# Performance work log

Measured on AMD Instinct MI355X. Metric: run time of the kernel, lower is better.

## Reference

```python
import jax, jax.numpy as jnp
import numpy as np

B, L, D, H = 2, 2048, 512, 8
DH = D // H
THRESHOLD = 0.1


def setup_inputs() -> dict:
    key = jax.random.key(0)
    ks = jax.random.split(key, 8)
    s = 0.02  # weight scale to keep activations sane
    return {
        "q_x": jax.random.normal(ks[0], (B, L, D), jnp.float32),
        "k_x": jax.random.normal(ks[1], (B, L, D), jnp.float32),
        "v_x": jax.random.normal(ks[2], (B, L, D), jnp.float32),
        "energy_coeffs": jax.random.normal(ks[3], (B, L, 16), jnp.float32),
        "Wq": jax.random.normal(ks[4], (D, D), jnp.float32) * s,
        "bq": jnp.zeros((D,), jnp.float32),
        "Wk": jax.random.normal(ks[5], (D, D), jnp.float32) * s,
        "bk": jnp.zeros((D,), jnp.float32),
        "Wv": jax.random.normal(ks[6], (D, D), jnp.float32) * s,
        "bv": jnp.zeros((D,), jnp.float32),
        "Wo": jax.random.normal(ks[7], (D, D), jnp.float32) * s,
        "bo": jnp.zeros((D,), jnp.float32),
    }


def reference(q_x, k_x, v_x, energy_coeffs, Wq, bq, Wk, bk, Wv, bv, Wo, bo):
    b, l, d = q_x.shape
    # QKV projections (torch Linear: x @ W.T + b), split heads -> [B,H,L,Dh]
    Q = (q_x @ Wq.T + bq).reshape(b, l, H, DH).transpose(0, 2, 1, 3)
    K = (k_x @ Wk.T + bk).reshape(b, -1, H, DH).transpose(0, 2, 1, 3)
    V = (v_x @ Wv.T + bv).reshape(b, -1, H, DH).transpose(0, 2, 1, 3)
    scores = jnp.einsum("bhqd,bhkd->bhqk", Q, K) / jnp.sqrt(jnp.float32(DH))
    # straight-through energy-based key mask
    energy = jnp.abs(energy_coeffs).mean(axis=-1)  # [B, Lk]
    soft = jax.nn.sigmoid((energy - THRESHOLD) * 10.0)
    hard = (energy > THRESHOLD).astype(q_x.dtype)
    mask_val = soft + jax.lax.stop_gradient(hard - soft)  # fwd=hard, grad=soft
    scores = scores + (1.0 - mask_val)[:, None, None, :] * (-1e9)
    attn = jax.nn.softmax(scores, axis=-1)
    out = jnp.einsum("bhqk,bhkd->bhqd", attn, V)
    out = out.transpose(0, 2, 1, 3).reshape(b, l, d)
    return out @ Wo.T + bo
```

## Files before the change

### kernel.cpp

```cpp
#include <hip/hip_runtime.h>
#include <stdint.h>

#define B_ 2
#define L_ 2048
#define D_ 512
#define H_ 8
#define DH_ 64

using frag8 = __attribute__((ext_vector_type(8))) short;
using bf4   = __attribute__((ext_vector_type(4))) short;
using f32x4 = __attribute__((ext_vector_type(4))) float;
using u32x4 = __attribute__((ext_vector_type(4))) unsigned int;

#define QSC 0.18033688011112042f

__device__ __forceinline__ unsigned short f2bf(float f) {
    unsigned int u = __float_as_uint(f);
    u += 0x7fffu + ((u >> 16) & 1u);
    return (unsigned short)(u >> 16);
}

__device__ __forceinline__ unsigned int cvtpk(float lo, float hi_) {
    unsigned int r;
    asm("v_cvt_pk_bf16_f32 %0, %1, %2" : "=v"(r) : "v"(lo), "v"(hi_));
    return r;
}

__device__ __forceinline__ void gl2lds16(const void* g, void* lds) {
    __builtin_amdgcn_global_load_lds((const __attribute__((address_space(1))) void*)g,
                                     (__attribute__((address_space(3))) void*)lds,
                                     16, 0, 0);
}

template<int N>
__device__ __forceinline__ void vmwait() {
    asm volatile("s_waitcnt vmcnt(%0)" :: "n"(N) : "memory");
}

__global__ __launch_bounds__(256) void cvt_mask_kernel(
    const float* __restrict__ qx, const float* __restrict__ kx, const float* __restrict__ vx,
    const float* __restrict__ Wq, const float* __restrict__ Wk, const float* __restrict__ Wv,
    const float* __restrict__ Wo, const float* __restrict__ ec,
    unsigned short* qb, unsigned short* kb, unsigned short* vb,
    unsigned short* wqb, unsigned short* wkb, unsigned short* wvb, unsigned short* wob,
    float* __restrict__ mk)
{
    const long NA = (long)B_ * L_ * D_;
    const long NW = (long)D_ * D_;
    const long total4 = (3 * NA + 4 * NW) / 4;
    long q4 = (long)blockIdx.x * 256 + threadIdx.x;
    if (q4 < total4) {
        long i = q4 * 4;
        const float* src; unsigned short* dst; long off;
        if (i < NA)            { src = qx; dst = qb; off = i; }
        else if (i < 2 * NA)   { src = kx; dst = kb; off = i - NA; }
        else if (i < 3 * NA)   { src = vx; dst = vb; off = i - 2 * NA; }
        else {
            long j = i - 3 * NA;
            int w = (int)(j / NW);
            off = j - (long)w * NW;
            src = (w == 0) ? Wq : (w == 1) ? Wk : (w == 2) ? Wv : Wo;
            dst = (w == 0) ? wqb : (w == 1) ? wkb : (w == 2) ? wvb : wob;
        }
        float4 v = *(const float4*)(src + off);
        ushort4 o;
        o.x = f2bf(v.x); o.y = f2bf(v.y); o.z = f2bf(v.z); o.w = f2bf(v.w);
        *(ushort4*)(dst + off) = o;
    } else {
        long i = q4 - total4;
        if (i < B_ * L_) {
            const float4* p4 = (const float4*)(ec + i * 16);
            float s = 0.0f;
#pragma unroll
            for (int j = 0; j < 4; ++j) {
                float4 v = p4[j];
                s += fabsf(v.x) + fabsf(v.y) + fabsf(v.z) + fabsf(v.w);
            }
            float energy = s * (1.0f / 16.0f);
            mk[i] = (energy > 0.1f) ? 0.0f : -1.0e9f;
        }
    }
}

struct GemmArgs { const unsigned short* A; const unsigned short* W;
                  const float* bias; void* C; int mode; };

template<int BM, int BN>
__global__ __launch_bounds__(256) void gemm_kernel(GemmArgs a0, GemmArgs a1, GemmArgs a2,
                                                   int M, int N, int K)
{
    const int nwg = gridDim.x * gridDim.y * gridDim.z;
    int flat = blockIdx.x + gridDim.x * (blockIdx.y + gridDim.y * blockIdx.z);
    int swz  = (flat & 7) * (nwg >> 3) + (flat >> 3);
    const int bx = swz % gridDim.x;
    int t2 = swz / gridDim.x;
    const int by = t2 % gridDim.y;
    const int bz = t2 / gridDim.y;

    GemmArgs ga = bz == 0 ? a0 : (bz == 1 ? a1 : a2);
    const unsigned short* __restrict__ A = ga.A;
    const unsigned short* __restrict__ W = ga.W;
    const float* __restrict__ bias = ga.bias;

    constexpr int MF = BM / 32;
    constexpr int NF = BN / 32;
    constexpr int NL = BM / 32 + BN / 32;

    __shared__ __align__(16) unsigned short As[2][BM * 64];
    __shared__ __align__(16) unsigned short Bs[2][BN * 64];

    const int tid  = threadIdx.x;
    const int lane = tid & 63;
    const int wave = tid >> 6;
    const int hi   = lane >> 4;
    const int ln   = lane & 15;
    const int wr   = wave >> 1;
    const int wc   = wave & 1;

    const long mBase = (long)by * BM;
    const long nBase = (long)bx * BN;

    f32x4 acc[MF][NF];
#pragma unroll
    for (int m = 0; m < MF; ++m)
#pragma unroll
        for (int n = 0; n < NF; ++n) acc[m][n] = (f32x4){0.f, 0.f, 0.f, 0.f};

#define GSTAGE(KT, BUF) do {                                                    \
    _Pragma("unroll")                                                           \
    for (int i_ = 0; i_ < BM / 32; ++i_) {                                      \
        int cl_ = i_ * 256 + tid;                                               \
        int r_ = cl_ >> 3, c_ = cl_ & 7, s_ = c_ ^ (r_ & 7);                    \
        gl2lds16(A + (mBase + r_) * K + (KT) + s_ * 8, As[BUF] + cl_ * 8);      \
    }                                                                           \
    _Pragma("unroll")                                                           \
    for (int i_ = 0; i_ < BN / 32; ++i_) {                                      \
        int cl_ = i_ * 256 + tid;                                               \
        int r_ = cl_ >> 3, c_ = cl_ & 7, s_ = c_ ^ (r_ & 7);                    \
        gl2lds16(W + (nBase + r_) * K + (KT) + s_ * 8, Bs[BUF] + cl_ * 8);      \
    }                                                                           \
} while (0)

    GSTAGE(0, 0);

    const int nk = K / 64;
    for (int t = 0; t < nk; ++t) {
        const int buf = t & 1;
        if (t + 1 < nk) {
            GSTAGE((t + 1) * 64, buf ^ 1);
            vmwait<NL>();
        } else {
            vmwait<0>();
        }
        __builtin_amdgcn_s_barrier();
        __builtin_amdgcn_sched_barrier(0);

        frag8 af[2][MF], bfr[2][NF];
#pragma unroll
        for (int kk = 0; kk < 2; ++kk) {
#pragma unroll
            for (int m = 0; m < MF; ++m) {
                int row = wr * (BM / 2) + m * 16 + ln;
                int c = (kk * 4 + hi) ^ (row & 7);
                af[kk][m] = *(const frag8*)(As[buf] + row * 64 + c * 8);
            }
#pragma unroll
            for (int n = 0; n < NF; ++n) {
                int row = wc * (BN / 2) + n * 16 + ln;
                int c = (kk * 4 + hi) ^ (row & 7);
                bfr[kk][n] = *(const frag8*)(Bs[buf] + row * 64 + c * 8);
            }
        }
        __builtin_amdgcn_s_setprio(1);
#pragma unroll
        for (int kk = 0; kk < 2; ++kk)
#pragma unroll
            for (int m = 0; m < MF; ++m)
#pragma unroll
                for (int n = 0; n < NF; ++n)
                    acc[m][n] = __builtin_amdgcn_mfma_f32_16x16x32_bf16(af[kk][m], bfr[kk][n], acc[m][n], 0, 0, 0);
        __builtin_amdgcn_s_setprio(0);
        __builtin_amdgcn_sched_barrier(0);
        __builtin_amdgcn_s_barrier();
    }
#undef GSTAGE

    const int mode = ga.mode;
#pragma unroll
    for (int m = 0; m < MF; ++m) {
#pragma unroll
        for (int n = 0; n < NF; ++n) {
            long col = nBase + wc * (BN / 2) + n * 16 + ln;
            float bv = bias[col];
#pragma unroll
            for (int j = 0; j < 4; ++j) {
                long row = mBase + wr * (BM / 2) + m * 16 + hi * 4 + j;
                float v = acc[m][n][j] + bv;
                if (mode == 3) {
                    ((float*)ga.C)[row * N + col] = v;
                } else if (mode == 2) {
                    int dh = (int)col & 63;
                    int swv = ((dh & 7) << 1) | ((dh >> 3) & 1);
                    long nt = (row & ~63L) | (long)(((((int)(row >> 2)) & 15) ^ swv) << 2) | (row & 3);
                    ((unsigned short*)ga.C)[col * (long)(B_ * L_) + nt] = f2bf(v);
                } else {
                    if (mode == 1) v *= QSC;
                    ((unsigned short*)ga.C)[row * N + col] = f2bf(v);
                }
            }
        }
    }
}

__global__ __launch_bounds__(512, 4) void attn_kernel(
    const unsigned short* __restrict__ Qg, const unsigned short* __restrict__ Kg,
    const unsigned short* __restrict__ Vt, const float* __restrict__ mkg,
    unsigned short* __restrict__ Og)
{
    const int tid  = threadIdx.x;
    const int lane = tid & 63;
    const int wave = tid >> 6;
    const int grp  = wave >> 2;
    const int wq   = wave & 3;
    const int gtid = tid & 255;
    const int hi   = lane >> 4;
    const int ln   = lane & 15;

    const int bh = blockIdx.y;
    const int b  = bh >> 3, h = bh & 7;
    const unsigned short* Qb = Qg + ((long)b * L_) * D_ + h * DH_;
    const unsigned short* Kb = Kg + ((long)b * L_) * D_ + h * DH_;
    const unsigned short* Vb = Vt + (long)(h * DH_) * (B_ * L_) + (long)b * L_;
    const float* mkb = mkg + (long)b * L_;

    __shared__ __align__(16) char smem[65536];
    unsigned short* KsG = (unsigned short*)(smem + grp * 32768);
    unsigned short* VsG = (unsigned short*)(smem + grp * 32768 + 16384);

    const int q0 = blockIdx.x * 64 + wq * 16;

    frag8 qf[2];
#pragma unroll
    for (int ks = 0; ks < 2; ++ks)
        qf[ks] = *(const frag8*)(Qb + (long)(q0 + ln) * D_ + ks * 32 + hi * 8);

    const int sw  = ((ln & 7) << 1) | ((ln >> 3) & 1);
    const int sl0 = ((hi     ) ^ sw) << 2;
    const int sl1 = ((hi + 4 ) ^ sw) << 2;
    const int sl2 = ((hi + 8 ) ^ sw) << 2;
    const int sl3 = ((hi + 12) ^ sw) << 2;

#define STAGE(TT, BUF) do {                                                     \
    _Pragma("unroll")                                                           \
    for (int c2_ = 0; c2_ < 2; ++c2_) {                                         \
        int cl_ = c2_ * 256 + gtid;                                             \
        int r_ = cl_ >> 3, c_ = cl_ & 7;                                        \
        gl2lds16(Kb + (long)((TT) * 64 + r_) * D_ + ((c_ ^ (r_ & 7)) << 3),     \
                 KsG + (BUF) * 4096 + cl_ * 8);                                 \
        gl2lds16(Vb + (long)r_ * (B_ * L_) + (TT) * 64 + (c_ << 3),             \
                 VsG + (BUF) * 4096 + cl_ * 8);                                 \
    }                                                                           \
} while (0)

    STAGE(grp, 0);

    f32x4 o[4];
#pragma unroll
    for (int g = 0; g < 4; ++g) o[g] = (f32x4){0.f, 0.f, 0.f, 0.f};
    float m_run = -__builtin_inff();
    float l_run = 0.0f;

    for (int i = 0; i < 16; ++i) {
        const int T = 2 * i + grp;
        const int buf = i & 1;

        float4 m40 = *(const float4*)(mkb + T * 64 +      4 * hi);
        float4 m41 = *(const float4*)(mkb + T * 64 + 16 + 4 * hi);
        float4 m42 = *(const float4*)(mkb + T * 64 + 32 + 4 * hi);
        float4 m43 = *(const float4*)(mkb + T * 64 + 48 + 4 * hi);
        __builtin_amdgcn_sched_barrier(0);

        if (i < 15) {
            STAGE(2 * (i + 1) + grp, buf ^ 1);
            vmwait<8>();
        } else {
            vmwait<4>();
        }
        __builtin_amdgcn_s_barrier();
        __builtin_amdgcn_sched_barrier(0);

        const unsigned short* Kl = KsG + buf * 4096;
        const unsigned short* Vl = VsG + buf * 4096;

        f32x4 sv[4];
#pragma unroll
        for (int sh = 0; sh < 4; ++sh) sv[sh] = (f32x4){0.f, 0.f, 0.f, 0.f};
        __builtin_amdgcn_s_setprio(1);
#pragma unroll
        for (int sh = 0; sh < 4; ++sh) {
            int key = sh * 16 + ln;
#pragma unroll
            for (int ks = 0; ks < 2; ++ks) {
                frag8 kf = *(const frag8*)(Kl + key * 64 + (((ks * 4 + hi) ^ (ln & 7)) << 3));
                sv[sh] = __builtin_amdgcn_mfma_f32_16x16x32_bf16(kf, qf[ks], sv[sh], 0, 0, 0);
            }
        }
        __builtin_amdgcn_s_setprio(0);

        float sc[16];
        sc[0]  = sv[0][0] + m40.x; sc[1]  = sv[0][1] + m40.y;
        sc[2]  = sv[0][2] + m40.z; sc[3]  = sv[0][3] + m40.w;
        sc[4]  = sv[1][0] + m41.x; sc[5]  = sv[1][1] + m41.y;
        sc[6]  = sv[1][2] + m41.z; sc[7]  = sv[1][3] + m41.w;
        sc[8]  = sv[2][0] + m42.x; sc[9]  = sv[2][1] + m42.y;
        sc[10] = sv[2][2] + m42.z; sc[11] = sv[2][3] + m42.w;
        sc[12] = sv[3][0] + m43.x; sc[13] = sv[3][1] + m43.y;
        sc[14] = sv[3][2] + m43.z; sc[15] = sv[3][3] + m43.w;

        float t0 = fmaxf(fmaxf(sc[0], sc[1]), sc[2]);
        float t1 = fmaxf(fmaxf(sc[3], sc[4]), sc[5]);
        float t2 = fmaxf(fmaxf(sc[6], sc[7]), sc[8]);
        float t3 = fmaxf(fmaxf(sc[9], sc[10]), sc[11]);
        float t4 = fmaxf(fmaxf(sc[12], sc[13]), sc[14]);
        float tmax = fmaxf(fmaxf(fmaxf(t0, t1), fmaxf(t2, t3)), fmaxf(t4, sc[15]));
        tmax = fmaxf(tmax, __shfl_xor(tmax, 16));
        tmax = fmaxf(tmax, __shfl_xor(tmax, 32));

        if (!__all(tmax <= m_run)) {
            float m_new = fmaxf(m_run, tmax);
            float alpha = __builtin_amdgcn_exp2f(m_run - m_new);
            float a0 = __shfl(alpha, 4 * hi + 0);
            float a1 = __shfl(alpha, 4 * hi + 1);
            float a2 = __shfl(alpha, 4 * hi + 2);
            float a3 = __shfl(alpha, 4 * hi + 3);
#pragma unroll
            for (int g = 0; g < 4; ++g) {
                o[g][0] *= a0; o[g][1] *= a1; o[g][2] *= a2; o[g][3] *= a3;
            }
            l_run *= alpha;
            m_run = m_new;
        }

        float p[16];
#pragma unroll
        for (int j = 0; j < 16; ++j) p[j] = __builtin_amdgcn_exp2f(sc[j] - m_run);
        float s01 = (p[0] + p[1]) + (p[2] + p[3]);
        float s23 = (p[4] + p[5]) + (p[6] + p[7]);
        float s45 = (p[8] + p[9]) + (p[10] + p[11]);
        float s67 = (p[12] + p[13]) + (p[14] + p[15]);
        float ps = (s01 + s23) + (s45 + s67);
        ps += __shfl_xor(ps, 16);
        ps += __shfl_xor(ps, 32);
        l_run += ps;

        union PU { u32x4 u; frag8 f; } p0u, p1u;
        p0u.u = (u32x4){cvtpk(p[0], p[1]),  cvtpk(p[2], p[3]),
                        cvtpk(p[4], p[5]),  cvtpk(p[6], p[7])};
        p1u.u = (u32x4){cvtpk(p[8], p[9]),  cvtpk(p[10], p[11]),
                        cvtpk(p[12], p[13]), cvtpk(p[14], p[15])};

        __builtin_amdgcn_s_setprio(1);
#pragma unroll
        for (int g = 0; g < 4; ++g) {
            int rowb = (g * 16 + ln) * 64;
            bf4 a0 = *(const bf4*)(Vl + rowb + sl0);
            bf4 a1 = *(const bf4*)(Vl + rowb + sl1);
            bf4 a2 = *(const bf4*)(Vl + rowb + sl2);
            bf4 a3 = *(const bf4*)(Vl + rowb + sl3);
            frag8 vf0 = __builtin_shufflevector(a0, a1, 0, 1, 2, 3, 4, 5, 6, 7);
            frag8 vf1 = __builtin_shufflevector(a2, a3, 0, 1, 2, 3, 4, 5, 6, 7);
            o[g] = __builtin_amdgcn_mfma_f32_16x16x32_bf16(p0u.f, vf0, o[g], 0, 0, 0);
            o[g] = __builtin_amdgcn_mfma_f32_16x16x32_bf16(p1u.f, vf1, o[g], 0, 0, 0);
        }
        __builtin_amdgcn_s_setprio(0);

        __builtin_amdgcn_sched_barrier(0);
        __builtin_amdgcn_s_barrier();
    }
#undef STAGE

    float* oX = (float*)smem;
    float* mX = (float*)(smem + 64 * 68 * 4);
    float* lX = mX + 64;

    if (grp == 1) {
#pragma unroll
        for (int g = 0; g < 4; ++g)
#pragma unroll
            for (int j = 0; j < 4; ++j)
                oX[(wq * 16 + 4 * hi + j) * 68 + g * 16 + ln] = o[g][j];
        if (hi == 0) { mX[wq * 16 + ln] = m_run; lX[wq * 16 + ln] = l_run; }
    }
    __syncthreads();
    if (grp == 0) {
#pragma unroll
        for (int j = 0; j < 4; ++j) {
            int q = 4 * hi + j;
            float mA = __shfl(m_run, q);
            float lA = __shfl(l_run, q);
            float mB = mX[wq * 16 + q];
            float lB = lX[wq * 16 + q];
            float mm = fmaxf(mA, mB);
            float aA = __builtin_amdgcn_exp2f(mA - mm);
            float aB = __builtin_amdgcn_exp2f(mB - mm);
            float inv = 1.0f / (lA * aA + lB * aB);
            aA *= inv; aB *= inv;
#pragma unroll
            for (int g = 0; g < 4; ++g) {
                float v = o[g][j] * aA + oX[(wq * 16 + q) * 68 + g * 16 + ln] * aB;
                long idx = ((long)b * L_ + q0 + q) * D_ + h * DH_ + g * 16 + ln;
                Og[idx] = f2bf(v);
            }
        }
    }
}

extern "C" void kernel_launch(void* const* d_in, const int* in_sizes, int n_in,
                              void* d_out, int out_size, void* d_ws, size_t ws_size,
                              hipStream_t stream)
{
    const float* qx = (const float*)d_in[0];
    const float* kx = (const float*)d_in[1];
    const float* vx = (const float*)d_in[2];
    const float* ec = (const float*)d_in[3];
    const float* Wq = (const float*)d_in[4];
    const float* bq = (const float*)d_in[5];
    const float* Wk = (const float*)d_in[6];
    const float* bk = (const float*)d_in[7];
    const float* Wv = (const float*)d_in[8];
    const float* bv = (const float*)d_in[9];
    const float* Wo = (const float*)d_in[10];
    const float* bo = (const float*)d_in[11];
    float* out = (float*)d_out;

    const long NA = (long)B_ * L_ * D_;
    const long NW = (long)D_ * D_;

    unsigned short* qb  = (unsigned short*)d_ws;
    unsigned short* kb  = qb + NA;
    unsigned short* vb  = kb + NA;
    unsigned short* wqb = vb + NA;
    unsigned short* wkb = wqb + NW;
    unsigned short* wvb = wkb + NW;
    unsigned short* wob = wvb + NW;
    unsigned short* Qp  = wob + NW;
    unsigned short* Kp  = Qp + NA;
    unsigned short* Vtp = Kp + NA;
    unsigned short* Ap  = qb;
    float*          mk  = (float*)(Vtp + NA);

    const long total4 = (3 * NA + 4 * NW) / 4;
    const long nblk = (total4 + B_ * L_ + 255) / 256;
    cvt_mask_kernel<<<dim3((unsigned)nblk), dim3(256), 0, stream>>>(
        qx, kx, vx, Wq, Wk, Wv, Wo, ec, qb, kb, vb, wqb, wkb, wvb, wob, mk);

    GemmArgs zq = {qb, wqb, bq, Qp, 1};
    GemmArgs zk = {kb, wkb, bk, Kp, 0};
    GemmArgs zv = {vb, wvb, bv, Vtp, 2};
    gemm_kernel<64, 128><<<dim3(4, 64, 3), dim3(256), 0, stream>>>(zq, zk, zv, B_ * L_, D_, D_);

    attn_kernel<<<dim3(L_ / 64, B_ * H_), dim3(512), 0, stream>>>(Qp, Kp, Vtp, mk, Ap);

    GemmArgs zo = {Ap, wob, bo, out, 3};
    gemm_kernel<64, 64><<<dim3(8, 64, 1), dim3(256), 0, stream>>>(zo, zo, zo, B_ * L_, D_, D_);
}
```

Baseline: 79.43 us.

## Drop split-KV groups in attention, use 256-thread blocks with lazy rescale

The attention kernel no longer splits keys between two 4-wave groups that are merged through LDS. Each 256-thread block now processes all 32 key tiles itself, using a 32KB double buffer and writing the normalized output directly. The V transpose swizzle is changed so each B fragment is fetched with two 16-byte LDS reads instead of four 8-byte reads. Max rescaling is now skipped unless the tile max exceeds the running max by more than 8, which trades a small risk of exp overflow for fewer rescales. The cost is twice as many serial iterations per block, offset by potentially higher occupancy and no final cross-group merge.

```diff
diff --git a/kernel.cpp b/kernel.cpp
--- a/kernel.cpp
+++ b/kernel.cpp
@@ -8,7 +8,6 @@
 #define DH_ 64
 
 using frag8 = __attribute__((ext_vector_type(8))) short;
-using bf4   = __attribute__((ext_vector_type(4))) short;
 using f32x4 = __attribute__((ext_vector_type(4))) float;
 using u32x4 = __attribute__((ext_vector_type(4))) unsigned int;
 
@@ -200,8 +199,10 @@
                     ((float*)ga.C)[row * N + col] = v;
                 } else if (mode == 2) {
                     int dh = (int)col & 63;
-                    int swv = ((dh & 7) << 1) | ((dh >> 3) & 1);
-                    long nt = (row & ~63L) | (long)(((((int)(row >> 2)) & 15) ^ swv) << 2) | (row & 3);
+                    int s  = ((int)row >> 2) & 15;
+                    int w  = (int)row & 3;
+                    int q  = ((((s & 3) << 2) | (s >> 2)) ^ ((dh & 7) << 1));
+                    long nt = (row & ~63L) | (long)(q << 2) | w;
                     ((unsigned short*)ga.C)[col * (long)(B_ * L_) + nt] = f2bf(v);
                 } else {
                     if (mode == 1) v *= QSC;
@@ -212,7 +213,7 @@
     }
 }
 
-__global__ __launch_bounds__(512, 4) void attn_kernel(
+__global__ __launch_bounds__(256, 5) void attn_kernel(
     const unsigned short* __restrict__ Qg, const unsigned short* __restrict__ Kg,
     const unsigned short* __restrict__ Vt, const float* __restrict__ mkg,
     unsigned short* __restrict__ Og)
@@ -220,9 +221,6 @@
     const int tid  = threadIdx.x;
     const int lane = tid & 63;
     const int wave = tid >> 6;
-    const int grp  = wave >> 2;
-    const int wq   = wave & 3;
-    const int gtid = tid & 255;
     const int hi   = lane >> 4;
     const int ln   = lane & 15;
 
@@ -233,36 +231,33 @@
     const unsigned short* Vb = Vt + (long)(h * DH_) * (B_ * L_) + (long)b * L_;
     const float* mkb = mkg + (long)b * L_;
 
-    __shared__ __align__(16) char smem[65536];
-    unsigned short* KsG = (unsigned short*)(smem + grp * 32768);
-    unsigned short* VsG = (unsigned short*)(smem + grp * 32768 + 16384);
-
-    const int q0 = blockIdx.x * 64 + wq * 16;
+    __shared__ __align__(16) unsigned short Ks[2][4096];
+    __shared__ __align__(16) unsigned short Vs[2][4096];
+
+    const int q0 = blockIdx.x * 64 + wave * 16;
 
     frag8 qf[2];
 #pragma unroll
     for (int ks = 0; ks < 2; ++ks)
         qf[ks] = *(const frag8*)(Qb + (long)(q0 + ln) * D_ + ks * 32 + hi * 8);
 
-    const int sw  = ((ln & 7) << 1) | ((ln >> 3) & 1);
-    const int sl0 = ((hi     ) ^ sw) << 2;
-    const int sl1 = ((hi + 4 ) ^ sw) << 2;
-    const int sl2 = ((hi + 8 ) ^ sw) << 2;
-    const int sl3 = ((hi + 12) ^ sw) << 2;
+    const int xv   = (ln & 7) << 1;
+    const int off0 = (((hi << 2) ^ xv)) << 2;
+    const int off1 = off0 ^ 8;
 
 #define STAGE(TT, BUF) do {                                                     \
     _Pragma("unroll")                                                           \
     for (int c2_ = 0; c2_ < 2; ++c2_) {                                         \
-        int cl_ = c2_ * 256 + gtid;                                             \
+        int cl_ = c2_ * 256 + tid;                                              \
         int r_ = cl_ >> 3, c_ = cl_ & 7;                                        \
         gl2lds16(Kb + (long)((TT) * 64 + r_) * D_ + ((c_ ^ (r_ & 7)) << 3),     \
-                 KsG + (BUF) * 4096 + cl_ * 8);                                 \
+                 Ks[BUF] + cl_ * 8);                                            \
         gl2lds16(Vb + (long)r_ * (B_ * L_) + (TT) * 64 + (c_ << 3),             \
-                 VsG + (BUF) * 4096 + cl_ * 8);                                 \
+                 Vs[BUF] + cl_ * 8);                                            \
     }                                                                           \
 } while (0)
 
-    STAGE(grp, 0);
+    STAGE(0, 0);
 
     f32x4 o[4];
 #pragma unroll
@@ -270,18 +265,18 @@
     float m_run = -__builtin_inff();
     float l_run = 0.0f;
 
-    for (int i = 0; i < 16; ++i) {
-        const int T = 2 * i + grp;
+#pragma unroll 2
+    for (int i = 0; i < 32; ++i) {
         const int buf = i & 1;
 
-        float4 m40 = *(const float4*)(mkb + T * 64 +      4 * hi);
-        float4 m41 = *(const float4*)(mkb + T * 64 + 16 + 4 * hi);
-        float4 m42 = *(const float4*)(mkb + T * 64 + 32 + 4 * hi);
-        float4 m43 = *(const float4*)(mkb + T * 64 + 48 + 4 * hi);
+        float4 m40 = *(const float4*)(mkb + i * 64 +      4 * hi);
+        float4 m41 = *(const float4*)(mkb + i * 64 + 16 + 4 * hi);
+        float4 m42 = *(const float4*)(mkb + i * 64 + 32 + 4 * hi);
+        float4 m43 = *(const float4*)(mkb + i * 64 + 48 + 4 * hi);
         __builtin_amdgcn_sched_barrier(0);
 
-        if (i < 15) {
-            STAGE(2 * (i + 1) + grp, buf ^ 1);
+        if (i < 31) {
+            STAGE(i + 1, buf ^ 1);
             vmwait<8>();
         } else {
             vmwait<4>();
@@ -289,8 +284,8 @@
         __builtin_amdgcn_s_barrier();
         __builtin_amdgcn_sched_barrier(0);
 
-        const unsigned short* Kl = KsG + buf * 4096;
-        const unsigned short* Vl = VsG + buf * 4096;
+        const unsigned short* Kl = Ks[buf];
+        const unsigned short* Vl = Vs[buf];
 
         f32x4 sv[4];
 #pragma unroll
@@ -317,16 +312,17 @@
         sc[12] = sv[3][0] + m43.x; sc[13] = sv[3][1] + m43.y;
         sc[14] = sv[3][2] + m43.z; sc[15] = sv[3][3] + m43.w;
 
-        float t0 = fmaxf(fmaxf(sc[0], sc[1]), sc[2]);
-        float t1 = fmaxf(fmaxf(sc[3], sc[4]), sc[5]);
-        float t2 = fmaxf(fmaxf(sc[6], sc[7]), sc[8]);
-        float t3 = fmaxf(fmaxf(sc[9], sc[10]), sc[11]);
-        float t4 = fmaxf(fmaxf(sc[12], sc[13]), sc[14]);
-        float tmax = fmaxf(fmaxf(fmaxf(t0, t1), fmaxf(t2, t3)), fmaxf(t4, sc[15]));
-        tmax = fmaxf(tmax, __shfl_xor(tmax, 16));
-        tmax = fmaxf(tmax, __shfl_xor(tmax, 32));
-
-        if (!__all(tmax <= m_run)) {
+        float t0 = fmaxf(fmaxf(sc[0], sc[1]), fmaxf(sc[2], sc[3]));
+        float t1 = fmaxf(fmaxf(sc[4], sc[5]), fmaxf(sc[6], sc[7]));
+        float t2 = fmaxf(fmaxf(sc[8], sc[9]), fmaxf(sc[10], sc[11]));
+        float t3 = fmaxf(fmaxf(sc[12], sc[13]), fmaxf(sc[14], sc[15]));
+        float tl = fmaxf(fmaxf(t0, t1), fmaxf(t2, t3));
+        float tA = __shfl_xor(tl, 16);
+        float tB = __shfl_xor(tl, 32);
+        float tC = __shfl_xor(tl, 48);
+        float tmax = fmaxf(fmaxf(tl, tA), fmaxf(tB, tC));
+
+        if (!__all(tmax <= m_run + 8.0f)) {
             float m_new = fmaxf(m_run, tmax);
             float alpha = __builtin_amdgcn_exp2f(m_run - m_new);
             float a0 = __shfl(alpha, 4 * hi + 0);
@@ -349,9 +345,10 @@
         float s45 = (p[8] + p[9]) + (p[10] + p[11]);
         float s67 = (p[12] + p[13]) + (p[14] + p[15]);
         float ps = (s01 + s23) + (s45 + s67);
-        ps += __shfl_xor(ps, 16);
-        ps += __shfl_xor(ps, 32);
-        l_run += ps;
+        float pA = __shfl_xor(ps, 16);
+        float pB = __shfl_xor(ps, 32);
+        float pC = __shfl_xor(ps, 48);
+        l_run += (ps + pA) + (pB + pC);
 
         union PU { u32x4 u; frag8 f; } p0u, p1u;
         p0u.u = (u32x4){cvtpk(p[0], p[1]),  cvtpk(p[2], p[3]),
@@ -362,13 +359,9 @@
         __builtin_amdgcn_s_setprio(1);
 #pragma unroll
         for (int g = 0; g < 4; ++g) {
-            int rowb = (g * 16 + ln) * 64;
-            bf4 a0 = *(const bf4*)(Vl + rowb + sl0);
-            bf4 a1 = *(const bf4*)(Vl + rowb + sl1);
-            bf4 a2 = *(const bf4*)(Vl + rowb + sl2);
-            bf4 a3 = *(const bf4*)(Vl + rowb + sl3);
-            frag8 vf0 = __builtin_shufflevector(a0, a1, 0, 1, 2, 3, 4, 5, 6, 7);
-            frag8 vf1 = __builtin_shufflevector(a2, a3, 0, 1, 2, 3, 4, 5, 6, 7);
+            int base = (g * 16 + ln) * 64;
+            frag8 vf0 = *(const frag8*)(Vl + base + off0);
+            frag8 vf1 = *(const frag8*)(Vl + base + off1);
             o[g] = __builtin_amdgcn_mfma_f32_16x16x32_bf16(p0u.f, vf0, o[g], 0, 0, 0);
             o[g] = __builtin_amdgcn_mfma_f32_16x16x32_bf16(p1u.f, vf1, o[g], 0, 0, 0);
         }
@@ -379,38 +372,18 @@
     }
 #undef STAGE
 
-    float* oX = (float*)smem;
-    float* mX = (float*)(smem + 64 * 68 * 4);
-    float* lX = mX + 64;
-
-    if (grp == 1) {
-#pragma unroll
-        for (int g = 0; g < 4; ++g)
-#pragma unroll
-            for (int j = 0; j < 4; ++j)
-                oX[(wq * 16 + 4 * hi + j) * 68 + g * 16 + ln] = o[g][j];
-        if (hi == 0) { mX[wq * 16 + ln] = m_run; lX[wq * 16 + ln] = l_run; }
-    }
-    __syncthreads();
-    if (grp == 0) {
+    float li = 1.0f / l_run;
+    float i0 = __shfl(li, 4 * hi + 0);
+    float i1 = __shfl(li, 4 * hi + 1);
+    float i2 = __shfl(li, 4 * hi + 2);
+    float i3 = __shfl(li, 4 * hi + 3);
+#pragma unroll
+    for (int g = 0; g < 4; ++g) {
+        const float iv[4] = {i0, i1, i2, i3};
 #pragma unroll
         for (int j = 0; j < 4; ++j) {
-            int q = 4 * hi + j;
-            float mA = __shfl(m_run, q);
-            float lA = __shfl(l_run, q);
-            float mB = mX[wq * 16 + q];
-            float lB = lX[wq * 16 + q];
-            float mm = fmaxf(mA, mB);
-            float aA = __builtin_amdgcn_exp2f(mA - mm);
-            float aB = __builtin_amdgcn_exp2f(mB - mm);
-            float inv = 1.0f / (lA * aA + lB * aB);
-            aA *= inv; aB *= inv;
-#pragma unroll
-            for (int g = 0; g < 4; ++g) {
-                float v = o[g][j] * aA + oX[(wq * 16 + q) * 68 + g * 16 + ln] * aB;
-                long idx = ((long)b * L_ + q0 + q) * D_ + h * DH_ + g * 16 + ln;
-                Og[idx] = f2bf(v);
-            }
+            long idx = ((long)b * L_ + q0 + 4 * hi + j) * D_ + h * DH_ + g * 16 + ln;
+            Og[idx] = f2bf(o[g][j] * iv[j]);
         }
     }
 }
@@ -459,7 +432,7 @@
     GemmArgs zv = {vb, wvb, bv, Vtp, 2};
     gemm_kernel<64, 128><<<dim3(4, 64, 3), dim3(256), 0, stream>>>(zq, zk, zv, B_ * L_, D_, D_);
 
-    attn_kernel<<<dim3(L_ / 64, B_ * H_), dim3(512), 0, stream>>>(Qp, Kp, Vtp, mk, Ap);
+    attn_kernel<<<dim3(L_ / 64, B_ * H_), dim3(256), 0, stream>>>(Qp, Kp, Vtp, mk, Ap);
 
     GemmArgs zo = {Ap, wob, bo, out, 3};
     gemm_kernel<64, 64><<<dim3(8, 64, 1), dim3(256), 0, stream>>>(zo, zo, zo, B_ * L_, D_, D_);
```

New measurement: 91.73 us. 15.5% more time.
